# Kernel optimization log

Hardware: AMD Instinct MI355X
Metric: run time of the kernel (lower is better)

The kernel has to match this reference:

```python
import jax, jax.numpy as jnp
import numpy as np

B, NQ, NKV, D = 16, 256, 256, 64


def setup_inputs() -> dict:
    key = jax.random.key(0)
    k1, k2, k3, k4, k5 = jax.random.split(key, 5)
    return {
        "v_equi": jax.random.normal(k1, (B, NKV, 3, D), dtype=jnp.float32),
        "messages": jax.random.normal(k2, (B, NQ, NKV, D), dtype=jnp.float32),
        "adj_mask": jax.random.randint(k3, (B, NQ, NKV), 0, 2, dtype=jnp.int32),
        "W_coord": jax.random.normal(k4, (D, D), dtype=jnp.float32) / np.sqrt(D),
        "W_attn": jax.random.normal(k5, (D, D), dtype=jnp.float32) / np.sqrt(D),
    }


def reference(v_equi, messages, adj_mask, W_coord, W_attn):
    adj = adj_mask.astype(bool)                              # [B,Nq,Nkv]
    # adj_to_attn_mask: -inf where no edge, but rows with no edges at all -> 0
    mask = jnp.where(adj, 0.0, -jnp.inf).astype(jnp.float32)
    row_empty = ~jnp.any(adj, axis=-1)                       # [B,Nq]
    mask = jnp.where(row_empty[..., None], 0.0, mask)
    # coord_proj (Linear, no bias): y = x @ W^T over last dim
    proj_equi = v_equi @ W_coord.T                           # [B,Nkv,3,D]
    # masked softmax over N_kv (dim=2), per equi channel d
    attn = jax.nn.softmax(messages + mask[..., None], axis=2)  # [B,Nq,Nkv,D]
    # batched skinny bmm over (B, d): [Nq,Nkv] @ [Nkv,3]
    attn_out = jnp.einsum("bqkd,bkcd->bqcd", attn, proj_equi)  # [B,Nq,3,D]
    # L2 norm of attention rows as a scale
    weights = jnp.sqrt(jnp.sum(attn * attn, axis=2))           # [B,Nq,D]
    attn_out = attn_out * weights[:, :, None, :]
    # attn_proj
    return attn_out @ W_attn.T                                 # [B,Nq,3,D]
```

## Files before the change

kernel.cpp:

```cpp
#include <hip/hip_runtime.h>
#include <math.h>

#define B_   16
#define NQ_  256
#define NKV_ 256
#define D_   64

__global__ __launch_bounds__(256) void rowmat_kernel(
    const float* __restrict__ in, const float* __restrict__ W,
    float* __restrict__ out)
{
    __shared__ float WT[64 * 65];
    __shared__ float vrow[4][64];

    int tid = threadIdx.x;
    for (int i = tid; i < 4096; i += 256)
        WT[(i & 63) * 65 + (i >> 6)] = W[i];

    int r = tid >> 6, d = tid & 63;
    size_t row0 = (size_t)blockIdx.x * 4;
    vrow[r][d] = in[row0 * 64 + tid];
    __syncthreads();

    float acc = 0.f;
#pragma unroll
    for (int e = 0; e < 64; ++e)
        acc = fmaf(vrow[r][e], WT[e * 65 + d], acc);
    out[(row0 + r) * 64 + d] = acc;
}

__global__ __launch_bounds__(256, 4) void attn_kernel(
    const float* __restrict__ messages, const int* __restrict__ adj,
    const float* __restrict__ proj, float* __restrict__ aout)
{
    __shared__ float red[4][5][64];
    __shared__ int   sadj[NKV_];
    __shared__ int   anyw[4];

    int tid  = threadIdx.x;
    int bq   = blockIdx.x;
    int lane = tid & 63, w = tid >> 6;

    int a = adj[(size_t)bq * NKV_ + tid];
    sadj[tid] = a;
    unsigned long long bal = __ballot(a != 0);
    if (lane == 0) anyw[w] = (bal != 0ULL) ? 1 : 0;
    __syncthreads();
    bool row_empty = (anyw[0] | anyw[1] | anyw[2] | anyw[3]) == 0;

    int dq = tid & 15;
    int kg = tid >> 4;

    const float4* mbase = (const float4*)(messages + (size_t)bq * NKV_ * D_);
    const float4* pbase = (const float4*)(proj + (size_t)(bq >> 8) * NKV_ * 3 * D_);

    float4 S  = make_float4(0.f, 0.f, 0.f, 0.f);
    float4 SS = make_float4(0.f, 0.f, 0.f, 0.f);
    float4 D0 = make_float4(0.f, 0.f, 0.f, 0.f);
    float4 D1 = make_float4(0.f, 0.f, 0.f, 0.f);
    float4 D2 = make_float4(0.f, 0.f, 0.f, 0.f);

#pragma unroll 4
    for (int i = 0; i < 16; ++i) {
        int k = i * 16 + kg;
        float4 m = mbase[k * 16 + dq];
        float wm = (sadj[k] != 0 || row_empty) ? 1.f : 0.f;
        float4 p;
        p.x = __expf(m.x) * wm; p.y = __expf(m.y) * wm;
        p.z = __expf(m.z) * wm; p.w = __expf(m.w) * wm;

        float4 p0 = pbase[k * 48 + dq];
        float4 p1 = pbase[k * 48 + 16 + dq];
        float4 p2 = pbase[k * 48 + 32 + dq];

        S.x += p.x;  S.y += p.y;  S.z += p.z;  S.w += p.w;
        SS.x = fmaf(p.x, p.x, SS.x); SS.y = fmaf(p.y, p.y, SS.y);
        SS.z = fmaf(p.z, p.z, SS.z); SS.w = fmaf(p.w, p.w, SS.w);
        D0.x = fmaf(p.x, p0.x, D0.x); D0.y = fmaf(p.y, p0.y, D0.y);
        D0.z = fmaf(p.z, p0.z, D0.z); D0.w = fmaf(p.w, p0.w, D0.w);
        D1.x = fmaf(p.x, p1.x, D1.x); D1.y = fmaf(p.y, p1.y, D1.y);
        D1.z = fmaf(p.z, p1.z, D1.z); D1.w = fmaf(p.w, p1.w, D1.w);
        D2.x = fmaf(p.x, p2.x, D2.x); D2.y = fmaf(p.y, p2.y, D2.y);
        D2.z = fmaf(p.z, p2.z, D2.z); D2.w = fmaf(p.w, p2.w, D2.w);
    }

    float vals[20] = { S.x, S.y, S.z, S.w,  SS.x, SS.y, SS.z, SS.w,
                       D0.x, D0.y, D0.z, D0.w, D1.x, D1.y, D1.z, D1.w,
                       D2.x, D2.y, D2.z, D2.w };
#pragma unroll
    for (int j = 0; j < 20; ++j) {
        vals[j] += __shfl_xor(vals[j], 16, 64);
        vals[j] += __shfl_xor(vals[j], 32, 64);
    }
    if (lane < 16) {
#pragma unroll
        for (int q = 0; q < 5; ++q)
            *(float4*)&red[w][q][dq * 4] =
                make_float4(vals[q*4], vals[q*4+1], vals[q*4+2], vals[q*4+3]);
    }
    __syncthreads();

    if (tid < 64) {
        int d = tid;
        float s = 0.f, ss = 0.f, e0 = 0.f, e1 = 0.f, e2 = 0.f;
#pragma unroll
        for (int w2 = 0; w2 < 4; ++w2) {
            s  += red[w2][0][d];
            ss += red[w2][1][d];
            e0 += red[w2][2][d];
            e1 += red[w2][3][d];
            e2 += red[w2][4][d];
        }
        float inv = 1.f / s;
        float scale = sqrtf(ss) * inv * inv;
        float* ab = aout + (size_t)bq * 3 * 64;
        ab[d]       = e0 * scale;
        ab[64 + d]  = e1 * scale;
        ab[128 + d] = e2 * scale;
    }
}

extern "C" void kernel_launch(void* const* d_in, const int* in_sizes, int n_in,
                              void* d_out, int out_size, void* d_ws, size_t ws_size,
                              hipStream_t stream) {
    const float* v_equi   = (const float*)d_in[0];
    const float* messages = (const float*)d_in[1];
    const int*   adj      = (const int*)d_in[2];
    const float* W_coord  = (const float*)d_in[3];
    const float* W_attn   = (const float*)d_in[4];
    float* out  = (float*)d_out;

    float* proj = (float*)d_ws;
    float* ao   = proj + (size_t)B_ * NKV_ * 3 * D_;

    rowmat_kernel<<<(B_ * NKV_ * 3) / 4, 256, 0, stream>>>(v_equi, W_coord, proj);
    attn_kernel<<<B_ * NQ_, 256, 0, stream>>>(messages, adj, proj, ao);
    rowmat_kernel<<<(B_ * NQ_ * 3) / 4, 256, 0, stream>>>(ao, W_attn, out);
}
```

Baseline: 419.4 us.

## Tile 16 queries per block and stage projected values in shared memory

The attention kernel now handles 16 query rows of one batch per block instead of one row. Each 64-key tile of the projected values is loaded once into LDS and reused by all 16 queries, which cuts the repeated global/L2 reads of proj. Each 16-thread group now owns one query row and covers all keys, so the cross-wave shuffle and shared-memory reduction are gone. The cost is a grid of only 256 blocks with launch bounds of one block per SM, so far fewer waves are available to hide the latency of streaming the messages.

```diff
diff --git a/kernel.cpp b/kernel.cpp
--- a/kernel.cpp
+++ b/kernel.cpp
@@ -5,6 +5,8 @@
 #define NQ_  256
 #define NKV_ 256
 #define D_   64
+#define TQ   16
+#define TK   64
 
 __global__ __launch_bounds__(256) void rowmat_kernel(
     const float* __restrict__ in, const float* __restrict__ W,
@@ -29,30 +31,36 @@
     out[(row0 + r) * 64 + d] = acc;
 }
 
-__global__ __launch_bounds__(256, 4) void attn_kernel(
+__global__ __launch_bounds__(256, 1) void attn_kernel(
     const float* __restrict__ messages, const int* __restrict__ adj,
     const float* __restrict__ proj, float* __restrict__ aout)
 {
-    __shared__ float red[4][5][64];
-    __shared__ int   sadj[NKV_];
-    __shared__ int   anyw[4];
+    __shared__ float sproj[TK * 3 * 64];
+    __shared__ unsigned char smask[TQ][NKV_];
+    __shared__ int rowany[TQ];
 
-    int tid  = threadIdx.x;
-    int bq   = blockIdx.x;
-    int lane = tid & 63, w = tid >> 6;
+    int tid = threadIdx.x;
+    int b   = blockIdx.x >> 4;
+    int q0  = (blockIdx.x & 15) * TQ;
 
-    int a = adj[(size_t)bq * NKV_ + tid];
-    sadj[tid] = a;
-    unsigned long long bal = __ballot(a != 0);
-    if (lane == 0) anyw[w] = (bal != 0ULL) ? 1 : 0;
+    if (tid < TQ) rowany[tid] = 0;
     __syncthreads();
-    bool row_empty = (anyw[0] | anyw[1] | anyw[2] | anyw[3]) == 0;
 
+    const int* abase = adj + ((size_t)b * NQ_ + q0) * NKV_;
+    for (int c = 0; c < TQ; ++c) {
+        int a = abase[c * NKV_ + tid];
+        smask[c][tid] = (a != 0) ? 1 : 0;
+        unsigned long long bal = __ballot(a != 0);
+        if ((tid & 63) == 0 && bal != 0ULL) atomicOr(&rowany[c], 1);
+    }
+    __syncthreads();
+
+    int q  = tid >> 4;
     int dq = tid & 15;
-    int kg = tid >> 4;
+    int re = (rowany[q] == 0) ? 1 : 0;
 
-    const float4* mbase = (const float4*)(messages + (size_t)bq * NKV_ * D_);
-    const float4* pbase = (const float4*)(proj + (size_t)(bq >> 8) * NKV_ * 3 * D_);
+    const float*  pb = proj + (size_t)b * NKV_ * 3 * D_;
+    const float4* mb = (const float4*)(messages + ((size_t)b * NQ_ + q0 + q) * NKV_ * D_);
 
     float4 S  = make_float4(0.f, 0.f, 0.f, 0.f);
     float4 SS = make_float4(0.f, 0.f, 0.f, 0.f);
@@ -60,64 +68,51 @@
     float4 D1 = make_float4(0.f, 0.f, 0.f, 0.f);
     float4 D2 = make_float4(0.f, 0.f, 0.f, 0.f);
 
-#pragma unroll 4
-    for (int i = 0; i < 16; ++i) {
-        int k = i * 16 + kg;
-        float4 m = mbase[k * 16 + dq];
-        float wm = (sadj[k] != 0 || row_empty) ? 1.f : 0.f;
-        float4 p;
-        p.x = __expf(m.x) * wm; p.y = __expf(m.y) * wm;
-        p.z = __expf(m.z) * wm; p.w = __expf(m.w) * wm;
+    for (int t = 0; t < NKV_ / TK; ++t) {
+        __syncthreads();
+        const float4* ps  = (const float4*)(pb + (size_t)t * TK * 3 * D_);
+        float4*       sd4 = (float4*)sproj;
+#pragma unroll
+        for (int i = 0; i < (TK * 3 * 64 / 4) / 256; ++i)
+            sd4[i * 256 + tid] = ps[i * 256 + tid];
+        __syncthreads();
 
-        float4 p0 = pbase[k * 48 + dq];
-        float4 p1 = pbase[k * 48 + 16 + dq];
-        float4 p2 = pbase[k * 48 + 32 + dq];
+#pragma unroll 8
+        for (int j = 0; j < TK; ++j) {
+            int k = t * TK + j;
+            float4 m = mb[k * 16 + dq];
+            float wm = (smask[q][k] | re) ? 1.f : 0.f;
+            float4 p;
+            p.x = __expf(m.x) * wm; p.y = __expf(m.y) * wm;
+            p.z = __expf(m.z) * wm; p.w = __expf(m.w) * wm;
 
-        S.x += p.x;  S.y += p.y;  S.z += p.z;  S.w += p.w;
-        SS.x = fmaf(p.x, p.x, SS.x); SS.y = fmaf(p.y, p.y, SS.y);
-        SS.z = fmaf(p.z, p.z, SS.z); SS.w = fmaf(p.w, p.w, SS.w);
-        D0.x = fmaf(p.x, p0.x, D0.x); D0.y = fmaf(p.y, p0.y, D0.y);
-        D0.z = fmaf(p.z, p0.z, D0.z); D0.w = fmaf(p.w, p0.w, D0.w);
-        D1.x = fmaf(p.x, p1.x, D1.x); D1.y = fmaf(p.y, p1.y, D1.y);
-        D1.z = fmaf(p.z, p1.z, D1.z); D1.w = fmaf(p.w, p1.w, D1.w);
-        D2.x = fmaf(p.x, p2.x, D2.x); D2.y = fmaf(p.y, p2.y, D2.y);
-        D2.z = fmaf(p.z, p2.z, D2.z); D2.w = fmaf(p.w, p2.w, D2.w);
+            const float4* sp = (const float4*)(sproj + j * 192);
+            float4 p0 = sp[dq];
+            float4 p1 = sp[16 + dq];
+            float4 p2 = sp[32 + dq];
+
+            S.x += p.x;  S.y += p.y;  S.z += p.z;  S.w += p.w;
+            SS.x = fmaf(p.x, p.x, SS.x); SS.y = fmaf(p.y, p.y, SS.y);
+            SS.z = fmaf(p.z, p.z, SS.z); SS.w = fmaf(p.w, p.w, SS.w);
+            D0.x = fmaf(p.x, p0.x, D0.x); D0.y = fmaf(p.y, p0.y, D0.y);
+            D0.z = fmaf(p.z, p0.z, D0.z); D0.w = fmaf(p.w, p0.w, D0.w);
+            D1.x = fmaf(p.x, p1.x, D1.x); D1.y = fmaf(p.y, p1.y, D1.y);
+            D1.z = fmaf(p.z, p1.z, D1.z); D1.w = fmaf(p.w, p1.w, D1.w);
+            D2.x = fmaf(p.x, p2.x, D2.x); D2.y = fmaf(p.y, p2.y, D2.y);
+            D2.z = fmaf(p.z, p2.z, D2.z); D2.w = fmaf(p.w, p2.w, D2.w);
+        }
     }
 
-    float vals[20] = { S.x, S.y, S.z, S.w,  SS.x, SS.y, SS.z, SS.w,
-                       D0.x, D0.y, D0.z, D0.w, D1.x, D1.y, D1.z, D1.w,
-                       D2.x, D2.y, D2.z, D2.w };
-#pragma unroll
-    for (int j = 0; j < 20; ++j) {
-        vals[j] += __shfl_xor(vals[j], 16, 64);
-        vals[j] += __shfl_xor(vals[j], 32, 64);
-    }
-    if (lane < 16) {
-#pragma unroll
-        for (int q = 0; q < 5; ++q)
-            *(float4*)&red[w][q][dq * 4] =
-                make_float4(vals[q*4], vals[q*4+1], vals[q*4+2], vals[q*4+3]);
-    }
-    __syncthreads();
+    float4 sc;
+    sc.x = sqrtf(SS.x) / (S.x * S.x);
+    sc.y = sqrtf(SS.y) / (S.y * S.y);
+    sc.z = sqrtf(SS.z) / (S.z * S.z);
+    sc.w = sqrtf(SS.w) / (S.w * S.w);
 
-    if (tid < 64) {
-        int d = tid;
-        float s = 0.f, ss = 0.f, e0 = 0.f, e1 = 0.f, e2 = 0.f;
-#pragma unroll
-        for (int w2 = 0; w2 < 4; ++w2) {
-            s  += red[w2][0][d];
-            ss += red[w2][1][d];
-            e0 += red[w2][2][d];
-            e1 += red[w2][3][d];
-            e2 += red[w2][4][d];
-        }
-        float inv = 1.f / s;
-        float scale = sqrtf(ss) * inv * inv;
-        float* ab = aout + (size_t)bq * 3 * 64;
-        ab[d]       = e0 * scale;
-        ab[64 + d]  = e1 * scale;
-        ab[128 + d] = e2 * scale;
-    }
+    float4* ab = (float4*)(aout + ((size_t)b * NQ_ + q0 + q) * 3 * D_);
+    ab[dq]      = make_float4(D0.x * sc.x, D0.y * sc.y, D0.z * sc.z, D0.w * sc.w);
+    ab[16 + dq] = make_float4(D1.x * sc.x, D1.y * sc.y, D1.z * sc.z, D1.w * sc.w);
+    ab[32 + dq] = make_float4(D2.x * sc.x, D2.y * sc.y, D2.z * sc.z, D2.w * sc.w);
 }
 
 extern "C" void kernel_launch(void* const* d_in, const int* in_sizes, int n_in,
@@ -134,6 +129,6 @@
     float* ao   = proj + (size_t)B_ * NKV_ * 3 * D_;
 
     rowmat_kernel<<<(B_ * NKV_ * 3) / 4, 256, 0, stream>>>(v_equi, W_coord, proj);
-    attn_kernel<<<B_ * NQ_, 256, 0, stream>>>(messages, adj, proj, ao);
+    attn_kernel<<<B_ * (NQ_ / TQ), 256, 0, stream>>>(messages, adj, proj, ao);
     rowmat_kernel<<<(B_ * NQ_ * 3) / 4, 256, 0, stream>>>(ao, W_attn, out);
 }
```

After: 493.8 us. +17.7%, slower.

## Fuse output projection into attention kernel, one wave per query row

Applied to the files above, without the earlier changes.

The attention kernel now gives each wavefront a whole query row, so each block handles four rows. The adjacency mask becomes a ballot bitmask held in registers, and the cross-wave shared-memory reduction goes away. The W_attn projection is fused into the end of the attention kernel, which removes the third launch and the intermediate write and read. The first projection kernel now processes 16 rows per block, so W is reloaded less often. The cost is that every attention block transposes W_attn into shared memory, and each wave's loop is four times longer with fewer blocks in flight.

```diff
diff --git a/kernel.cpp b/kernel.cpp
--- a/kernel.cpp
+++ b/kernel.cpp
@@ -6,53 +6,60 @@
 #define NKV_ 256
 #define D_   64
 
-__global__ __launch_bounds__(256) void rowmat_kernel(
+__global__ __launch_bounds__(256) void rowmat16_kernel(
     const float* __restrict__ in, const float* __restrict__ W,
     float* __restrict__ out)
 {
     __shared__ float WT[64 * 65];
-    __shared__ float vrow[4][64];
+    __shared__ float vr[16][64];
 
     int tid = threadIdx.x;
     for (int i = tid; i < 4096; i += 256)
         WT[(i & 63) * 65 + (i >> 6)] = W[i];
 
-    int r = tid >> 6, d = tid & 63;
-    size_t row0 = (size_t)blockIdx.x * 4;
-    vrow[r][d] = in[row0 * 64 + tid];
+    size_t row0 = (size_t)blockIdx.x * 16;
+    ((float4*)&vr[0][0])[tid] = ((const float4*)(in + row0 * 64))[tid];
     __syncthreads();
 
-    float acc = 0.f;
+    int r4 = tid >> 6, d = tid & 63;
 #pragma unroll
-    for (int e = 0; e < 64; ++e)
-        acc = fmaf(vrow[r][e], WT[e * 65 + d], acc);
-    out[(row0 + r) * 64 + d] = acc;
+    for (int g = 0; g < 4; ++g) {
+        int r = g * 4 + r4;
+        float acc = 0.f;
+#pragma unroll
+        for (int e = 0; e < 64; ++e)
+            acc = fmaf(vr[r][e], WT[e * 65 + d], acc);
+        out[(row0 + r) * 64 + d] = acc;
+    }
 }
 
 __global__ __launch_bounds__(256, 4) void attn_kernel(
     const float* __restrict__ messages, const int* __restrict__ adj,
-    const float* __restrict__ proj, float* __restrict__ aout)
+    const float* __restrict__ proj, const float* __restrict__ W_attn,
+    float* __restrict__ out)
 {
-    __shared__ float red[4][5][64];
-    __shared__ int   sadj[NKV_];
-    __shared__ int   anyw[4];
+    __shared__ float WaT[64 * 65];
+    __shared__ float sao[4][3 * 64];
 
-    int tid  = threadIdx.x;
-    int bq   = blockIdx.x;
-    int lane = tid & 63, w = tid >> 6;
+    int tid = threadIdx.x;
+    for (int i = tid; i < 4096; i += 256)
+        WaT[(i & 63) * 65 + (i >> 6)] = W_attn[i];
 
-    int a = adj[(size_t)bq * NKV_ + tid];
-    sadj[tid] = a;
-    unsigned long long bal = __ballot(a != 0);
-    if (lane == 0) anyw[w] = (bal != 0ULL) ? 1 : 0;
-    __syncthreads();
-    bool row_empty = (anyw[0] | anyw[1] | anyw[2] | anyw[3]) == 0;
+    int w = tid >> 6, lane = tid & 63;
+    int sub = lane >> 4, dq = lane & 15;
+    size_t row = (size_t)blockIdx.x * 4 + w;
+    int b = (int)(row >> 8);
 
-    int dq = tid & 15;
-    int kg = tid >> 4;
+    int4 a4 = ((const int4*)(adj + row * NKV_))[lane];
+    unsigned long long b0 = __ballot(a4.x != 0);
+    unsigned long long b1 = __ballot(a4.y != 0);
+    unsigned long long b2 = __ballot(a4.z != 0);
+    unsigned long long b3 = __ballot(a4.w != 0);
+    unsigned long long mreg = (sub == 0) ? b0 : (sub == 1) ? b1 : (sub == 2) ? b2 : b3;
+    if ((b0 | b1 | b2 | b3) == 0ULL) mreg = ~0ULL;
 
-    const float4* mbase = (const float4*)(messages + (size_t)bq * NKV_ * D_);
-    const float4* pbase = (const float4*)(proj + (size_t)(bq >> 8) * NKV_ * 3 * D_);
+    const float4* mb = (const float4*)(messages + row * (NKV_ * D_));
+    const float4* pb = (const float4*)(proj + (size_t)b * NKV_ * 3 * D_);
 
     float4 S  = make_float4(0.f, 0.f, 0.f, 0.f);
     float4 SS = make_float4(0.f, 0.f, 0.f, 0.f);
@@ -61,17 +68,17 @@
     float4 D2 = make_float4(0.f, 0.f, 0.f, 0.f);
 
 #pragma unroll 4
-    for (int i = 0; i < 16; ++i) {
-        int k = i * 16 + kg;
-        float4 m = mbase[k * 16 + dq];
-        float wm = (sadj[k] != 0 || row_empty) ? 1.f : 0.f;
+    for (int i = 0; i < 64; ++i) {
+        int k = i * 4 + sub;
+        float4 m = mb[k * 16 + dq];
+        float wm = (float)((mreg >> i) & 1ULL);
         float4 p;
         p.x = __expf(m.x) * wm; p.y = __expf(m.y) * wm;
         p.z = __expf(m.z) * wm; p.w = __expf(m.w) * wm;
 
-        float4 p0 = pbase[k * 48 + dq];
-        float4 p1 = pbase[k * 48 + 16 + dq];
-        float4 p2 = pbase[k * 48 + 32 + dq];
+        float4 p0 = pb[k * 48 + dq];
+        float4 p1 = pb[k * 48 + 16 + dq];
+        float4 p2 = pb[k * 48 + 32 + dq];
 
         S.x += p.x;  S.y += p.y;  S.z += p.z;  S.w += p.w;
         SS.x = fmaf(p.x, p.x, SS.x); SS.y = fmaf(p.y, p.y, SS.y);
@@ -92,31 +99,29 @@
         vals[j] += __shfl_xor(vals[j], 16, 64);
         vals[j] += __shfl_xor(vals[j], 32, 64);
     }
-    if (lane < 16) {
+
+    if (sub == 0) {
+        float scx = sqrtf(vals[4]) / (vals[0] * vals[0]);
+        float scy = sqrtf(vals[5]) / (vals[1] * vals[1]);
+        float scz = sqrtf(vals[6]) / (vals[2] * vals[2]);
+        float scw = sqrtf(vals[7]) / (vals[3] * vals[3]);
 #pragma unroll
-        for (int q = 0; q < 5; ++q)
-            *(float4*)&red[w][q][dq * 4] =
-                make_float4(vals[q*4], vals[q*4+1], vals[q*4+2], vals[q*4+3]);
+        for (int c = 0; c < 3; ++c)
+            *(float4*)&sao[w][c * 64 + dq * 4] =
+                make_float4(vals[8 + c*4]     * scx, vals[8 + c*4 + 1] * scy,
+                            vals[8 + c*4 + 2] * scz, vals[8 + c*4 + 3] * scw);
     }
     __syncthreads();
 
-    if (tid < 64) {
-        int d = tid;
-        float s = 0.f, ss = 0.f, e0 = 0.f, e1 = 0.f, e2 = 0.f;
+    int r = tid >> 6, d = tid & 63;
+    size_t orow = (size_t)blockIdx.x * 4 + r;
 #pragma unroll
-        for (int w2 = 0; w2 < 4; ++w2) {
-            s  += red[w2][0][d];
-            ss += red[w2][1][d];
-            e0 += red[w2][2][d];
-            e1 += red[w2][3][d];
-            e2 += red[w2][4][d];
-        }
-        float inv = 1.f / s;
-        float scale = sqrtf(ss) * inv * inv;
-        float* ab = aout + (size_t)bq * 3 * 64;
-        ab[d]       = e0 * scale;
-        ab[64 + d]  = e1 * scale;
-        ab[128 + d] = e2 * scale;
+    for (int c = 0; c < 3; ++c) {
+        float acc = 0.f;
+#pragma unroll
+        for (int e = 0; e < 64; ++e)
+            acc = fmaf(sao[r][c * 64 + e], WaT[e * 65 + d], acc);
+        out[orow * 192 + c * 64 + d] = acc;
     }
 }
 
@@ -129,11 +134,8 @@
     const float* W_coord  = (const float*)d_in[3];
     const float* W_attn   = (const float*)d_in[4];
     float* out  = (float*)d_out;
+    float* proj = (float*)d_ws;
 
-    float* proj = (float*)d_ws;
-    float* ao   = proj + (size_t)B_ * NKV_ * 3 * D_;
-
-    rowmat_kernel<<<(B_ * NKV_ * 3) / 4, 256, 0, stream>>>(v_equi, W_coord, proj);
-    attn_kernel<<<B_ * NQ_, 256, 0, stream>>>(messages, adj, proj, ao);
-    rowmat_kernel<<<(B_ * NQ_ * 3) / 4, 256, 0, stream>>>(ao, W_attn, out);
+    rowmat16_kernel<<<(B_ * NKV_ * 3) / 16, 256, 0, stream>>>(v_equi, W_coord, proj);
+    attn_kernel<<<(B_ * NQ_) / 4, 256, 0, stream>>>(messages, adj, proj, W_attn, out);
 }
```

New measurement: 398.9 us. -4.9%, faster.
